# Kernel tuning notes

Hardware: AMD Instinct MI355X
Metric: run time of the kernel (lower is better)

Reference implementation:

```python
import jax, jax.numpy as jnp
import numpy as np

PAD = 1  # padding from init_kwargs

def setup_inputs() -> dict:
    key = jax.random.key(0)
    k1, k2 = jax.random.split(key)
    x = jax.random.normal(k1, (1, 256, 224, 224), dtype=jnp.float32)
    # Conv2d_mvm weight: [out_channels, in_channels, kh, kw]
    weight = jax.random.normal(k2, (256, 256, 3, 3), dtype=jnp.float32) * 0.05
    return {"x": x, "weight": weight}

def reference(x, weight):
    # Exact math of the bit-sliced crossbar conv forward: stride-1 cross-correlation
    # with zero padding, no bias, output squeezed to [C_out, H_out, W_out]
    # (the original forward emits no batch dimension).
    out = jax.lax.conv_general_dilated(
        x, weight,
        window_strides=(1, 1),
        padding=((PAD, PAD), (PAD, PAD)),
        dimension_numbers=("NCHW", "OIHW", "NCHW"),
    )
    return out[0]  # [C_out, H_out, W_out]
```

## Files before the change

### kernel.cpp

```cpp
#include <hip/hip_runtime.h>


#define H 224
#define W 224
#define NPOS (H*W)
#define CI 256
#define CO 256
#define KDIM 2304
#define HP 226
#define XP_ELEMS (HP*HP*CI)
#define AP_ELEMS (CO*KDIM)

typedef __bf16 bf16x8 __attribute__((ext_vector_type(8)));
typedef float f32x4 __attribute__((ext_vector_type(4)));
typedef unsigned short u16x4 __attribute__((ext_vector_type(4)));
typedef unsigned short u16x8 __attribute__((ext_vector_type(8)));
typedef float f32x4v __attribute__((ext_vector_type(4)));

__device__ __forceinline__ unsigned short f2bf(float f) {
    unsigned int u = __float_as_uint(f);
    u += 0x7fff + ((u >> 16) & 1);
    return (unsigned short)(u >> 16);
}

__device__ __forceinline__ void load_lds16(const unsigned short* g, unsigned short* l) {
    __builtin_amdgcn_global_load_lds(
        (const __attribute__((address_space(1))) void*)g,
        (__attribute__((address_space(3))) void*)l,
        16, 0, 0);
}

#define XT_BLOCKS 3136
#define WT_BLOCKS 256
#define BORDER_V8 28800
#define ROW_V8 7232
__global__ void prep_kernel(const float* __restrict__ x, const float* __restrict__ w,
                            unsigned short* __restrict__ ap, unsigned short* __restrict__ xp) {
    __shared__ unsigned short smem[64 * 68];
    const int bx = blockIdx.x;
    const int t = threadIdx.x;

    if (bx < XT_BLOCKS) {
        const unsigned int pBase = (unsigned int)(bx % 784) * 64;
        const unsigned int ciBase = (unsigned int)(bx / 784) * 64;
        {
            const int p4 = (t & 15) * 4;
            const int c0 = t >> 4;
#pragma unroll
            for (int i = 0; i < 4; ++i) {
                const int ci_l = c0 + i * 16;
                const f32x4 v = *(const f32x4*)&x[(ciBase + ci_l) * NPOS + pBase + p4];
                u16x4 s;
                s[0] = f2bf(v[0]); s[1] = f2bf(v[1]); s[2] = f2bf(v[2]); s[3] = f2bf(v[3]);
                *(u16x4*)&smem[ci_l * 68 + p4] = s;
            }
        }
        __syncthreads();
        {
            const int ci0 = (t & 7) * 8;
            const int pr = t >> 3;
#pragma unroll
            for (int j = 0; j < 2; ++j) {
                const int p_l = pr + j * 32;
                const unsigned int p = pBase + p_l;
                const unsigned int hi = p / W, wi = p - hi * W;
                u16x8 v;
#pragma unroll
                for (int k = 0; k < 8; ++k) v[k] = smem[(ci0 + k) * 68 + p_l];
                *(u16x8*)&xp[((hi + 1) * HP + (wi + 1)) * CI + ciBase + ci0] = v;
            }
        }
    } else if (bx < XT_BLOCKS + WT_BLOCKS) {
        const int co = bx - XT_BLOCKS;
        const float* wc = w + co * KDIM;
#pragma unroll
        for (int i = 0; i < 9; ++i)
            smem[i * 256 + t] = f2bf(wc[i * 256 + t]);
        __syncthreads();
        unsigned short* apc = ap + co * KDIM;
#pragma unroll
        for (int tap = 0; tap < 9; ++tap)
            apc[tap * 256 + t] = smem[t * 9 + tap];
    } else {
        const int idx = (bx - XT_BLOCKS - WT_BLOCKS) * 256 + t;
        if (idx < BORDER_V8) {
            unsigned short* p;
            if (idx < 2 * ROW_V8) {
                const int r = idx / ROW_V8;
                const int off = idx - r * ROW_V8;
                p = xp + r * (225 * HP * CI) + off * 8;
            } else {
                const int i2 = idx - 2 * ROW_V8;
                const int seg = i2 >> 5;
                const int o = i2 & 31;
                const int hp = 1 + (seg >> 1);
                const int wp = (seg & 1) * 225;
                p = xp + (hp * HP + wp) * CI + o * 8;
            }
            *(u16x8*)p = (u16x8){0, 0, 0, 0, 0, 0, 0, 0};
        }
    }
}

__global__ __launch_bounds__(256, 3) void gemm_conv_kernel(
    const unsigned short* __restrict__ Ap,
    const unsigned short* __restrict__ Xp,
    float* __restrict__ out)
{
    __shared__ unsigned short Als[2][4096];
    __shared__ unsigned short Bls[2][4096];

    const int tid = threadIdx.x;
    const int Nb = blockIdx.x;
    const int Mb = blockIdx.y;
    const int wave = tid >> 6;
    const int wm = wave >> 1;
    const int wn = wave & 1;
    const int lane = tid & 63;
    const int ln15 = lane & 15;
    const int quad = lane >> 4;
    const int sw = ln15 & 3;

    const int l2 = lane >> 2;
    const int c4 = (lane & 3) ^ (l2 & 3);

    const unsigned short* a_src[2];
    const unsigned short* b_src[2];
#pragma unroll
    for (int j = 0; j < 2; ++j) {
        const int row = (wave * 2 + j) * 16 + l2;
        a_src[j] = Ap + (Mb * 128 + row) * KDIM + c4 * 8;
        unsigned int p = Nb * 128 + row;
        unsigned int hi = p / W, wi = p - hi * W;
        b_src[j] = Xp + (hi * HP + wi) * CI + c4 * 8;
    }

    f32x4 acc[4][4];
#pragma unroll
    for (int mi = 0; mi < 4; ++mi)
#pragma unroll
        for (int ni = 0; ni < 4; ++ni)
            acc[mi][ni] = (f32x4){0.f, 0.f, 0.f, 0.f};

    auto stage = [&](int kc, int buf) {
        const int tap = kc >> 3;
        const int dh = tap / 3, dw = tap - dh * 3;
        const int boff = (dh * HP + dw) * CI + (kc & 7) * 32;
        const int aoff = kc * 32;
#pragma unroll
        for (int j = 0; j < 2; ++j) {
            load_lds16(a_src[j] + aoff, &Als[buf][(wave * 2 + j) * 512]);
            load_lds16(b_src[j] + boff, &Bls[buf][(wave * 2 + j) * 512]);
        }
    };

    stage(0, 0);
    __syncthreads();

    for (int kc = 0; kc < 72; ++kc) {
        const int cur = kc & 1;
        if (kc < 71) stage(kc + 1, cur ^ 1);

        bf16x8 af[4], bfr[4];
#pragma unroll
        for (int mi = 0; mi < 4; ++mi)
            af[mi] = *(const bf16x8*)&Als[cur][(wm * 64 + mi * 16 + ln15) * 32 +
                                              ((quad ^ sw) * 8)];
#pragma unroll
        for (int ni = 0; ni < 4; ++ni)
            bfr[ni] = *(const bf16x8*)&Bls[cur][(wn * 64 + ni * 16 + ln15) * 32 +
                                               ((quad ^ sw) * 8)];
#pragma unroll
        for (int mi = 0; mi < 4; ++mi)
#pragma unroll
            for (int ni = 0; ni < 4; ++ni)
                acc[mi][ni] = __builtin_amdgcn_mfma_f32_16x16x32_bf16(
                    af[mi], bfr[ni], acc[mi][ni], 0, 0, 0);

        __syncthreads();
    }

    const int pcol = Nb * 128 + wn * 64 + ln15;
    const int corow = Mb * 128 + wm * 64 + quad * 4;
#pragma unroll
    for (int mi = 0; mi < 4; ++mi)
#pragma unroll
        for (int ni = 0; ni < 4; ++ni)
#pragma unroll
            for (int r = 0; r < 4; ++r)
                out[(corow + mi * 16 + r) * NPOS + pcol + ni * 16] = acc[mi][ni][r];
}

extern "C" void kernel_launch(void* const* d_in, const int* in_sizes, int n_in,
                              void* d_out, int out_size, void* d_ws, size_t ws_size,
                              hipStream_t stream) {
    const float* x = (const float*)d_in[0];
    const float* w = (const float*)d_in[1];
    float* out = (float*)d_out;

    unsigned short* xp = (unsigned short*)d_ws;
    unsigned short* ap = xp + XP_ELEMS;

    prep_kernel<<<XT_BLOCKS + WT_BLOCKS + 113, 256, 0, stream>>>(x, w, ap, xp);
    gemm_conv_kernel<<<dim3(NPOS / 128, CO / 128), 256, 0, stream>>>(ap, xp, out);
}
```

Baseline: 180.6 us.

## Enlarge GEMM tile to 256x256 with 8 waves and triple-buffered LDS pipeline

The implicit-GEMM conv kernel now uses a 256x256 output tile per block (all output channels) with 512 threads and 8 waves, each computing 128x64. LDS goes from double to triple buffering, with loads issued two k-steps ahead, explicit vmcnt/lgkmcnt waits, split A/B staging interleaved between two MFMA halves, and s_setprio around MFMA bursts. This is meant to increase data reuse per loaded byte and overlap global loads with compute. In exchange, occupancy drops to one block per CU with large LDS and register use, and the hand-placed waits and barriers make correctness fragile.

```diff
diff --git a/kernel.cpp b/kernel.cpp
--- a/kernel.cpp
+++ b/kernel.cpp
@@ -15,7 +15,6 @@
 typedef float f32x4 __attribute__((ext_vector_type(4)));
 typedef unsigned short u16x4 __attribute__((ext_vector_type(4)));
 typedef unsigned short u16x8 __attribute__((ext_vector_type(8)));
-typedef float f32x4v __attribute__((ext_vector_type(4)));
 
 __device__ __forceinline__ unsigned short f2bf(float f) {
     unsigned int u = __float_as_uint(f);
@@ -102,88 +101,141 @@
     }
 }
 
-__global__ __launch_bounds__(256, 3) void gemm_conv_kernel(
+__global__ __launch_bounds__(512, 1) void gemm_conv_kernel(
     const unsigned short* __restrict__ Ap,
     const unsigned short* __restrict__ Xp,
     float* __restrict__ out)
 {
-    __shared__ unsigned short Als[2][4096];
-    __shared__ unsigned short Bls[2][4096];
+    __shared__ unsigned short Als[3][8192];
+    __shared__ unsigned short Bls[3][8192];
 
     const int tid = threadIdx.x;
     const int Nb = blockIdx.x;
-    const int Mb = blockIdx.y;
     const int wave = tid >> 6;
-    const int wm = wave >> 1;
-    const int wn = wave & 1;
+    const int wm = wave >> 2;
+    const int wn = wave & 3;
     const int lane = tid & 63;
     const int ln15 = lane & 15;
     const int quad = lane >> 4;
-    const int sw = ln15 & 3;
-
-    const int l2 = lane >> 2;
-    const int c4 = (lane & 3) ^ (l2 & 3);
+    const int xsw = ((quad ^ (ln15 & 3)) * 8);
+
+    const int rl = lane >> 2;
+    const int sc = (lane & 3) ^ (rl & 3);
 
     const unsigned short* a_src[2];
     const unsigned short* b_src[2];
 #pragma unroll
     for (int j = 0; j < 2; ++j) {
-        const int row = (wave * 2 + j) * 16 + l2;
-        a_src[j] = Ap + (Mb * 128 + row) * KDIM + c4 * 8;
-        unsigned int p = Nb * 128 + row;
+        const int row = j * 128 + wave * 16 + rl;
+        a_src[j] = Ap + row * KDIM + sc * 8;
+        unsigned int p = Nb * 256 + row;
         unsigned int hi = p / W, wi = p - hi * W;
-        b_src[j] = Xp + (hi * HP + wi) * CI + c4 * 8;
-    }
-
-    f32x4 acc[4][4];
-#pragma unroll
-    for (int mi = 0; mi < 4; ++mi)
+        b_src[j] = Xp + (hi * HP + wi) * CI + sc * 8;
+    }
+
+    f32x4 acc[8][4];
+#pragma unroll
+    for (int mi = 0; mi < 8; ++mi)
 #pragma unroll
         for (int ni = 0; ni < 4; ++ni)
             acc[mi][ni] = (f32x4){0.f, 0.f, 0.f, 0.f};
 
-    auto stage = [&](int kc, int buf) {
-        const int tap = kc >> 3;
+    auto stageA = [&](int kt, int buf) {
+        const int aoff = kt * 32;
+#pragma unroll
+        for (int j = 0; j < 2; ++j)
+            load_lds16(a_src[j] + aoff, &Als[buf][(j * 8 + wave) * 512]);
+    };
+    auto stageB = [&](int kt, int buf) {
+        const int tap = kt >> 3;
         const int dh = tap / 3, dw = tap - dh * 3;
-        const int boff = (dh * HP + dw) * CI + (kc & 7) * 32;
-        const int aoff = kc * 32;
-#pragma unroll
-        for (int j = 0; j < 2; ++j) {
-            load_lds16(a_src[j] + aoff, &Als[buf][(wave * 2 + j) * 512]);
-            load_lds16(b_src[j] + boff, &Bls[buf][(wave * 2 + j) * 512]);
-        }
-    };
-
-    stage(0, 0);
-    __syncthreads();
-
-    for (int kc = 0; kc < 72; ++kc) {
-        const int cur = kc & 1;
-        if (kc < 71) stage(kc + 1, cur ^ 1);
-
-        bf16x8 af[4], bfr[4];
+        const int boff = (dh * HP + dw) * CI + (kt & 7) * 32;
+#pragma unroll
+        for (int j = 0; j < 2; ++j)
+            load_lds16(b_src[j] + boff, &Bls[buf][(j * 8 + wave) * 512]);
+    };
+
+    bf16x8 af[4], bfr[4];
+    const int aBase = (wm * 128 + ln15) * 32 + xsw;
+    const int bBase = (wn * 64 + ln15) * 32 + xsw;
+
+    auto ldA = [&](int c, int half) {
 #pragma unroll
         for (int mi = 0; mi < 4; ++mi)
-            af[mi] = *(const bf16x8*)&Als[cur][(wm * 64 + mi * 16 + ln15) * 32 +
-                                              ((quad ^ sw) * 8)];
+            af[mi] = *(const bf16x8*)&Als[c][aBase + (half * 64 + mi * 16) * 32];
+    };
+    auto ldB = [&](int c) {
 #pragma unroll
         for (int ni = 0; ni < 4; ++ni)
-            bfr[ni] = *(const bf16x8*)&Bls[cur][(wn * 64 + ni * 16 + ln15) * 32 +
-                                               ((quad ^ sw) * 8)];
+            bfr[ni] = *(const bf16x8*)&Bls[c][bBase + ni * 16 * 32];
+    };
+    auto mfma16 = [&](int half) {
+        __builtin_amdgcn_s_setprio(1);
 #pragma unroll
         for (int mi = 0; mi < 4; ++mi)
 #pragma unroll
             for (int ni = 0; ni < 4; ++ni)
-                acc[mi][ni] = __builtin_amdgcn_mfma_f32_16x16x32_bf16(
-                    af[mi], bfr[ni], acc[mi][ni], 0, 0, 0);
-
-        __syncthreads();
-    }
-
-    const int pcol = Nb * 128 + wn * 64 + ln15;
-    const int corow = Mb * 128 + wm * 64 + quad * 4;
-#pragma unroll
-    for (int mi = 0; mi < 4; ++mi)
+                acc[half * 4 + mi][ni] = __builtin_amdgcn_mfma_f32_16x16x32_bf16(
+                    af[mi], bfr[ni], acc[half * 4 + mi][ni], 0, 0, 0);
+        __builtin_amdgcn_s_setprio(0);
+    };
+
+    stageA(0, 0); stageB(0, 0);
+    stageA(1, 1); stageB(1, 1);
+    asm volatile("s_waitcnt vmcnt(4)" ::: "memory");
+    __builtin_amdgcn_s_barrier();
+
+    int c = 0;
+    for (int kt = 0; kt < 70; ++kt) {
+        const int s = (c == 0) ? 2 : c - 1;
+        ldA(c, 0); ldB(c);
+        stageA(kt + 2, s);
+        __builtin_amdgcn_s_barrier();
+        asm volatile("s_waitcnt lgkmcnt(0)" ::: "memory");
+        __builtin_amdgcn_sched_barrier(0);
+        mfma16(0);
+        __builtin_amdgcn_s_barrier();
+        ldA(c, 1);
+        stageB(kt + 2, s);
+        asm volatile("s_waitcnt vmcnt(4)" ::: "memory");
+        __builtin_amdgcn_s_barrier();
+        asm volatile("s_waitcnt lgkmcnt(0)" ::: "memory");
+        __builtin_amdgcn_sched_barrier(0);
+        mfma16(1);
+        __builtin_amdgcn_s_barrier();
+        c = (c == 2) ? 0 : c + 1;
+    }
+    {
+        ldA(c, 0); ldB(c);
+        __builtin_amdgcn_s_barrier();
+        asm volatile("s_waitcnt lgkmcnt(0)" ::: "memory");
+        __builtin_amdgcn_sched_barrier(0);
+        mfma16(0);
+        __builtin_amdgcn_s_barrier();
+        ldA(c, 1);
+        asm volatile("s_waitcnt vmcnt(0)" ::: "memory");
+        __builtin_amdgcn_s_barrier();
+        asm volatile("s_waitcnt lgkmcnt(0)" ::: "memory");
+        __builtin_amdgcn_sched_barrier(0);
+        mfma16(1);
+        __builtin_amdgcn_s_barrier();
+        c = (c == 2) ? 0 : c + 1;
+    }
+    {
+        ldA(c, 0); ldB(c);
+        asm volatile("s_waitcnt lgkmcnt(0)" ::: "memory");
+        __builtin_amdgcn_sched_barrier(0);
+        mfma16(0);
+        ldA(c, 1);
+        asm volatile("s_waitcnt lgkmcnt(0)" ::: "memory");
+        __builtin_amdgcn_sched_barrier(0);
+        mfma16(1);
+    }
+
+    const int pcol = Nb * 256 + wn * 64 + ln15;
+    const int corow = wm * 128 + quad * 4;
+#pragma unroll
+    for (int mi = 0; mi < 8; ++mi)
 #pragma unroll
         for (int ni = 0; ni < 4; ++ni)
 #pragma unroll
@@ -202,5 +254,5 @@
     unsigned short* ap = xp + XP_ELEMS;
 
     prep_kernel<<<XT_BLOCKS + WT_BLOCKS + 113, 256, 0, stream>>>(x, w, ap, xp);
-    gemm_conv_kernel<<<dim3(NPOS / 128, CO / 128), 256, 0, stream>>>(ap, xp, out);
-}
+    gemm_conv_kernel<<<dim3(NPOS / 256), 512, 0, stream>>>(ap, xp, out);
+}
```

After: 187.2 us. +3.6%, slower.

## Triple-buffer LDS tiles with explicit vmcnt waits and MFMA priority boost

Applied to the files above, without the earlier changes.

The GEMM main loop moves from a double-buffered LDS pipeline with a full __syncthreads per k-step to a three-stage ring. Global-to-LDS loads are issued two steps ahead, and the code waits on them with explicit s_waitcnt vmcnt counts and raw s_barrier. The MFMA block is wrapped in s_setprio so waves doing math get issue priority. The aim is to hide global load latency better, at the cost of 50% more LDS per block, which may lower occupancy, and fragile hand-written wait counts.

```diff
diff --git a/kernel.cpp b/kernel.cpp
--- a/kernel.cpp
+++ b/kernel.cpp
@@ -15,7 +15,6 @@
 typedef float f32x4 __attribute__((ext_vector_type(4)));
 typedef unsigned short u16x4 __attribute__((ext_vector_type(4)));
 typedef unsigned short u16x8 __attribute__((ext_vector_type(8)));
-typedef float f32x4v __attribute__((ext_vector_type(4)));
 
 __device__ __forceinline__ unsigned short f2bf(float f) {
     unsigned int u = __float_as_uint(f);
@@ -107,8 +106,8 @@
     const unsigned short* __restrict__ Xp,
     float* __restrict__ out)
 {
-    __shared__ unsigned short Als[2][4096];
-    __shared__ unsigned short Bls[2][4096];
+    __shared__ unsigned short Als[3][4096];
+    __shared__ unsigned short Bls[3][4096];
 
     const int tid = threadIdx.x;
     const int Nb = blockIdx.x;
@@ -119,20 +118,20 @@
     const int lane = tid & 63;
     const int ln15 = lane & 15;
     const int quad = lane >> 4;
-    const int sw = ln15 & 3;
-
-    const int l2 = lane >> 2;
-    const int c4 = (lane & 3) ^ (l2 & 3);
+    const int xsw = (quad ^ (ln15 & 3)) * 8;
+
+    const int rl = lane >> 2;
+    const int sc = (lane & 3) ^ (rl & 3);
 
     const unsigned short* a_src[2];
     const unsigned short* b_src[2];
 #pragma unroll
     for (int j = 0; j < 2; ++j) {
-        const int row = (wave * 2 + j) * 16 + l2;
-        a_src[j] = Ap + (Mb * 128 + row) * KDIM + c4 * 8;
+        const int row = (wave * 2 + j) * 16 + rl;
+        a_src[j] = Ap + (Mb * 128 + row) * KDIM + sc * 8;
         unsigned int p = Nb * 128 + row;
         unsigned int hi = p / W, wi = p - hi * W;
-        b_src[j] = Xp + (hi * HP + wi) * CI + c4 * 8;
+        b_src[j] = Xp + (hi * HP + wi) * CI + sc * 8;
     }
 
     f32x4 acc[4][4];
@@ -142,11 +141,11 @@
         for (int ni = 0; ni < 4; ++ni)
             acc[mi][ni] = (f32x4){0.f, 0.f, 0.f, 0.f};
 
-    auto stage = [&](int kc, int buf) {
-        const int tap = kc >> 3;
+    auto stage = [&](int kt, int buf) {
+        const int tap = kt >> 3;
         const int dh = tap / 3, dw = tap - dh * 3;
-        const int boff = (dh * HP + dw) * CI + (kc & 7) * 32;
-        const int aoff = kc * 32;
+        const int boff = (dh * HP + dw) * CI + (kt & 7) * 32;
+        const int aoff = kt * 32;
 #pragma unroll
         for (int j = 0; j < 2; ++j) {
             load_lds16(a_src[j] + aoff, &Als[buf][(wave * 2 + j) * 512]);
@@ -154,30 +153,62 @@
         }
     };
 
-    stage(0, 0);
-    __syncthreads();
-
-    for (int kc = 0; kc < 72; ++kc) {
-        const int cur = kc & 1;
-        if (kc < 71) stage(kc + 1, cur ^ 1);
-
-        bf16x8 af[4], bfr[4];
+    bf16x8 af[4], bfr[4];
+    const int aBase = (wm * 64 + ln15) * 32 + xsw;
+    const int bBase = (wn * 64 + ln15) * 32 + xsw;
+
+    auto ldAB = [&](int c) {
 #pragma unroll
         for (int mi = 0; mi < 4; ++mi)
-            af[mi] = *(const bf16x8*)&Als[cur][(wm * 64 + mi * 16 + ln15) * 32 +
-                                              ((quad ^ sw) * 8)];
+            af[mi] = *(const bf16x8*)&Als[c][aBase + mi * 16 * 32];
 #pragma unroll
         for (int ni = 0; ni < 4; ++ni)
-            bfr[ni] = *(const bf16x8*)&Bls[cur][(wn * 64 + ni * 16 + ln15) * 32 +
-                                               ((quad ^ sw) * 8)];
+            bfr[ni] = *(const bf16x8*)&Bls[c][bBase + ni * 16 * 32];
+    };
+    auto mfma16 = [&]() {
+        __builtin_amdgcn_s_setprio(1);
 #pragma unroll
         for (int mi = 0; mi < 4; ++mi)
 #pragma unroll
             for (int ni = 0; ni < 4; ++ni)
                 acc[mi][ni] = __builtin_amdgcn_mfma_f32_16x16x32_bf16(
                     af[mi], bfr[ni], acc[mi][ni], 0, 0, 0);
-
-        __syncthreads();
+        __builtin_amdgcn_s_setprio(0);
+    };
+
+    stage(0, 0);
+    stage(1, 1);
+    asm volatile("s_waitcnt vmcnt(4)" ::: "memory");
+    __builtin_amdgcn_s_barrier();
+
+    int c = 0;
+    for (int kt = 0; kt < 70; ++kt) {
+        const int s = (c == 0) ? 2 : c - 1;
+        ldAB(c);
+        stage(kt + 2, s);
+        asm volatile("s_waitcnt vmcnt(4)" ::: "memory");
+        __builtin_amdgcn_s_barrier();
+        asm volatile("s_waitcnt lgkmcnt(0)" ::: "memory");
+        __builtin_amdgcn_sched_barrier(0);
+        mfma16();
+        __builtin_amdgcn_s_barrier();
+        c = (c == 2) ? 0 : c + 1;
+    }
+    {
+        ldAB(c);
+        asm volatile("s_waitcnt vmcnt(0)" ::: "memory");
+        __builtin_amdgcn_s_barrier();
+        asm volatile("s_waitcnt lgkmcnt(0)" ::: "memory");
+        __builtin_amdgcn_sched_barrier(0);
+        mfma16();
+        __builtin_amdgcn_s_barrier();
+        c = (c == 2) ? 0 : c + 1;
+    }
+    {
+        ldAB(c);
+        asm volatile("s_waitcnt lgkmcnt(0)" ::: "memory");
+        __builtin_amdgcn_sched_barrier(0);
+        mfma16();
     }
 
     const int pcol = Nb * 128 + wn * 64 + ln15;
```

New measurement: 187.9 us. 1.04x slower.
